# Performance work log

Hardware: AMD Instinct MI355X
Metric: run time of the kernel (lower is better)

The kernel has to match this reference:

```python
import jax, jax.numpy as jnp
import numpy as np

N = 100000   # nodes
E = 600000   # edges
SIZES = [128, 128, 128, 64]


def setup_inputs() -> dict:
    key = jax.random.key(0)
    ks = jax.random.split(key, 16)
    x = jax.random.normal(ks[0], (N, SIZES[0]), dtype=jnp.float32)
    edge_index = jax.random.randint(ks[1], (2, E), 0, N, dtype=jnp.int64)
    inp = {"x": x, "edge_index": edge_index}
    ki = 2
    for i in range(3):
        fin, fout = SIZES[i], SIZES[i + 1]
        s = 1.0 / np.sqrt(fin)
        inp[f"Wl{i}"] = jax.random.uniform(ks[ki], (fout, fin), jnp.float32, -s, s); ki += 1
        inp[f"bl{i}"] = jax.random.uniform(ks[ki], (fout,), jnp.float32, -s, s); ki += 1
        inp[f"Wr{i}"] = jax.random.uniform(ks[ki], (fout, fin), jnp.float32, -s, s); ki += 1
    return inp


def _sage(h, src, dst, Wl, bl, Wr):
    # PyG SAGEConv (aggr='mean'): out = lin_l(mean_{j in N(i)} x_j) + lin_r(x_i)
    msg_sum = jax.ops.segment_sum(h[src], dst, num_segments=N)          # [N, fin]
    cnt = jax.ops.segment_sum(jnp.ones((src.shape[0],), h.dtype), dst, num_segments=N)
    mean = msg_sum / jnp.maximum(cnt, 1.0)[:, None]                      # nodes w/o nbrs -> 0
    return mean @ Wl.T + bl + h @ Wr.T


def reference(x, edge_index, Wl0, bl0, Wr0, Wl1, bl1, Wr1, Wl2, bl2, Wr2):
    src, dst = edge_index[0], edge_index[1]
    h = _sage(x, src, dst, Wl0, bl0, Wr0)
    h = jax.nn.relu(h)                 # dropout p=0.0 -> identity
    h = _sage(h, src, dst, Wl1, bl1, Wr1)
    h = jax.nn.relu(h)
    h = _sage(h, src, dst, Wl2, bl2, Wr2)
    return h                            # last_layer='linear' appends nothing
```

## Files before the change

kernel.cpp:

```cpp
#include <hip/hip_runtime.h>

#define NN 100000
#define NE 600000
constexpr int FIN = 128;
constexpr int SCAN_BLOCKS = (NN + 255) / 256;

typedef __attribute__((ext_vector_type(8))) short bf16x8;
typedef __attribute__((ext_vector_type(4))) float f32x4;

__device__ __forceinline__ unsigned packbf2(float a, float b) {
  unsigned ua = __float_as_uint(a); ua += 0x7FFFu + ((ua >> 16) & 1u);
  unsigned ub = __float_as_uint(b); ub += 0x7FFFu + ((ub >> 16) & 1u);
  return (ua >> 16) | (ub & 0xFFFF0000u);
}
__device__ __forceinline__ float lo16f(unsigned u) { return __uint_as_float(u << 16); }
__device__ __forceinline__ float hi16f(unsigned u) { return __uint_as_float(u & 0xFFFF0000u); }

__device__ __forceinline__ void acc8(float* a, const uint4& v) {
  a[0] += lo16f(v.x); a[1] += hi16f(v.x);
  a[2] += lo16f(v.y); a[3] += hi16f(v.y);
  a[4] += lo16f(v.z); a[5] += hi16f(v.z);
  a[6] += lo16f(v.w); a[7] += hi16f(v.w);
}

template <int NCT>
__device__ __forceinline__ void castw_one(int pidx, const float* __restrict__ Wl,
                                          const float* __restrict__ Wr,
                                          short* __restrict__ wpk) {
  int t = pidx & 7;
  int lane = (pidx >> 3) & 63;
  int ks = (pidx >> 9) & 1;
  int c = (pidx >> 10) & (NCT - 1);
  int chunk = pidx >> ((NCT == 8) ? 13 : 12);
  int l15 = lane & 15, lq = lane >> 4;
  int j = c * 16 + l15;
  int k = chunk * 64 + ks * 32 + lq * 8 + t;
  float v = (k < 128) ? Wl[j * 128 + k] : Wr[j * 128 + (k - 128)];
  unsigned u = __float_as_uint(v);
  u += 0x7FFFu + ((u >> 16) & 1u);
  wpk[pidx] = (short)(u >> 16);
}

__global__ __launch_bounds__(256) void k_prep(
    const float* __restrict__ Wl0, const float* __restrict__ Wr0,
    const float* __restrict__ Wl1, const float* __restrict__ Wr1,
    const float* __restrict__ Wl2, const float* __restrict__ Wr2,
    short* __restrict__ wpk_all, float4* __restrict__ dc,
    const float* __restrict__ x, short* __restrict__ xb) {
  const int b = blockIdx.x;
  if (b < 320) {
    int pidx = b * 256 + threadIdx.x;
    if (pidx < 32768) castw_one<8>(pidx, Wl0, Wr0, wpk_all);
    else if (pidx < 65536) castw_one<8>(pidx - 32768, Wl1, Wr1, wpk_all + 32768);
    else castw_one<4>(pidx - 65536, Wl2, Wr2, wpk_all + 65536);
  } else if (b < 516) {
    int i = (b - 320) * 256 + threadIdx.x;
    if (i < 2 * NN / 4) dc[i] = make_float4(0.f, 0.f, 0.f, 0.f);
  } else {
    int i = (b - 516) * 256 + threadIdx.x;
    if (i < NN * FIN / 8) {
      const float4 v0 = *reinterpret_cast<const float4*>(x + (size_t)i * 8);
      const float4 v1 = *reinterpret_cast<const float4*>(x + (size_t)i * 8 + 4);
      uint4 o;
      o.x = packbf2(v0.x, v0.y);
      o.y = packbf2(v0.z, v0.w);
      o.z = packbf2(v1.x, v1.y);
      o.w = packbf2(v1.z, v1.w);
      *reinterpret_cast<uint4*>(xb + (size_t)i * 8) = o;
    }
  }
}


__global__ __launch_bounds__(256) void k_count(const int* __restrict__ dst,
                                               int* __restrict__ deg) {
  int e = blockIdx.x * blockDim.x + threadIdx.x;
  if (e < NE) {
    int d = dst[e];
    if ((unsigned)d < NN) atomicAdd(&deg[d], 1);
  }
}

__global__ __launch_bounds__(256) void k_scan1(const int* __restrict__ deg,
                                               int* __restrict__ rowptr,
                                               int* __restrict__ bsum,
                                               float* __restrict__ inv) {
  __shared__ int s[256];
  int i = blockIdx.x * 256 + threadIdx.x;
  int v = (i < NN) ? deg[i] : 0;
  s[threadIdx.x] = v;
  if (i < NN) inv[i] = 1.0f / fmaxf((float)v, 1.0f);
  __syncthreads();
#pragma unroll
  for (int off = 1; off < 256; off <<= 1) {
    int t = (threadIdx.x >= off) ? s[threadIdx.x - off] : 0;
    __syncthreads();
    s[threadIdx.x] += t;
    __syncthreads();
  }
  if (i < NN) rowptr[i + 1] = s[threadIdx.x];
  if (threadIdx.x == 255) bsum[blockIdx.x] = s[255];
}

__global__ __launch_bounds__(512) void k_scan2(int* __restrict__ bsum, int nb) {
  __shared__ int s[512];
  int v = (threadIdx.x < nb) ? bsum[threadIdx.x] : 0;
  s[threadIdx.x] = v;
  __syncthreads();
#pragma unroll
  for (int off = 1; off < 512; off <<= 1) {
    int t = (threadIdx.x >= off) ? s[threadIdx.x - off] : 0;
    __syncthreads();
    s[threadIdx.x] += t;
    __syncthreads();
  }
  if (threadIdx.x < nb) bsum[threadIdx.x] = s[threadIdx.x];
}

__global__ __launch_bounds__(256) void k_scan3(const int* __restrict__ bsum,
                                               int* __restrict__ rowptr) {
  int i = blockIdx.x * 256 + threadIdx.x;
  if (i < NN && blockIdx.x > 0) rowptr[i + 1] += bsum[blockIdx.x - 1];
  if (i == 0) rowptr[0] = 0;
}

__global__ __launch_bounds__(256) void k_fill(const int* __restrict__ src,
                                              const int* __restrict__ dst,
                                              const int* __restrict__ rowptr,
                                              int* __restrict__ cursor,
                                              int* __restrict__ adj) {
  int e = blockIdx.x * blockDim.x + threadIdx.x;
  if (e < NE) {
    int d = dst[e];
    int s = src[e];
    if ((unsigned)d < NN && (unsigned)s < NN) {
      int pos = atomicAdd(&cursor[d], 1);
      adj[rowptr[d] + pos] = s;
    }
  }
}

__global__ __launch_bounds__(256, 8) void k_gather2(
    const int* __restrict__ rowptr, const int* __restrict__ adj,
    const short* __restrict__ hb, const float* __restrict__ inv,
    short* __restrict__ mb) {
  const int node = blockIdx.x * 16 + (threadIdx.x >> 4);
  const int l15 = threadIdx.x & 15;
  if (node >= NN) return;
  const int beg = rowptr[node];
  const int end = rowptr[node + 1];
  const float s = inv[node];
  float a[8] = {0.f, 0.f, 0.f, 0.f, 0.f, 0.f, 0.f, 0.f};
  int e = beg;
  for (; e + 3 < end; e += 4) {
    int s0 = adj[e], s1 = adj[e + 1], s2 = adj[e + 2], s3 = adj[e + 3];
    uint4 v0 = *reinterpret_cast<const uint4*>(hb + (size_t)s0 * FIN + l15 * 8);
    uint4 v1 = *reinterpret_cast<const uint4*>(hb + (size_t)s1 * FIN + l15 * 8);
    uint4 v2 = *reinterpret_cast<const uint4*>(hb + (size_t)s2 * FIN + l15 * 8);
    uint4 v3 = *reinterpret_cast<const uint4*>(hb + (size_t)s3 * FIN + l15 * 8);
    acc8(a, v0); acc8(a, v1); acc8(a, v2); acc8(a, v3);
  }
  for (; e < end; ++e) {
    uint4 v = *reinterpret_cast<const uint4*>(hb + (size_t)adj[e] * FIN + l15 * 8);
    acc8(a, v);
  }
  uint4 o;
  o.x = packbf2(a[0] * s, a[1] * s);
  o.y = packbf2(a[2] * s, a[3] * s);
  o.z = packbf2(a[4] * s, a[5] * s);
  o.w = packbf2(a[6] * s, a[7] * s);
  *reinterpret_cast<uint4*>(mb + (size_t)node * FIN + l15 * 8) = o;
}

template <int FOUT, bool RELU, bool WF32, bool WB16>
__global__ __launch_bounds__(1024, 2) void k_gemm2(
    const short* __restrict__ hb, const short* __restrict__ mb,
    const short* __restrict__ wpk, const float* __restrict__ bias,
    float* __restrict__ out, short* __restrict__ outb) {
  constexpr int NCT = FOUT / 16;
  constexpr int NFR = NCT * 4 * 2;
  __shared__ short wlds[NFR * 64 * 8];
  const int lane = threadIdx.x & 63;
  const int w = threadIdx.x >> 6;
  const int l15 = lane & 15;
  const int lq = lane >> 4;
  const int n0 = (blockIdx.x * 16 + w) * 16;
  const int row = n0 + l15;
  const bool ok = row < NN;

#pragma unroll
  for (int i = 0; i < NFR / 16; ++i) {
    int idx = i * 1024 + threadIdx.x;
    reinterpret_cast<uint4*>(wlds)[idx] =
        reinterpret_cast<const uint4*>(wpk)[idx];
  }

  bf16x8 am[4], as_[4];
  {
    const short* mp = mb + (size_t)row * FIN + lq * 8;
    const short* sp = hb + (size_t)row * FIN + lq * 8;
#pragma unroll
    for (int q = 0; q < 4; ++q) {
      const int o = (q >> 1) * 64 + (q & 1) * 32;
      if (ok) {
        am[q] = *reinterpret_cast<const bf16x8*>(mp + o);
        as_[q] = *reinterpret_cast<const bf16x8*>(sp + o);
      } else {
#pragma unroll
        for (int i = 0; i < 8; ++i) { am[q][i] = 0; as_[q][i] = 0; }
      }
    }
  }

  __syncthreads();

  f32x4 acc[NCT];
#pragma unroll
  for (int c = 0; c < NCT; ++c)
#pragma unroll
    for (int q = 0; q < 4; ++q) acc[c][q] = 0.f;

#pragma unroll
  for (int chunk = 0; chunk < 4; ++chunk) {
    const bf16x8 a0 = (chunk < 2) ? am[chunk * 2 + 0] : as_[(chunk - 2) * 2 + 0];
    const bf16x8 a1 = (chunk < 2) ? am[chunk * 2 + 1] : as_[(chunk - 2) * 2 + 1];
#pragma unroll
    for (int c = 0; c < NCT; ++c) {
      const bf16x8 b0 = *reinterpret_cast<const bf16x8*>(
          &wlds[(((chunk * NCT + c) * 2 + 0) * 64 + lane) * 8]);
      const bf16x8 b1 = *reinterpret_cast<const bf16x8*>(
          &wlds[(((chunk * NCT + c) * 2 + 1) * 64 + lane) * 8]);
      acc[c] = __builtin_amdgcn_mfma_f32_16x16x32_bf16(b0, a0, acc[c], 0, 0, 0);
      acc[c] = __builtin_amdgcn_mfma_f32_16x16x32_bf16(b1, a1, acc[c], 0, 0, 0);
    }
  }

#pragma unroll
  for (int c = 0; c < NCT; ++c) {
    const f32x4 bb = *reinterpret_cast<const f32x4*>(bias + c * 16 + lq * 4);
    if (ok) {
      f32x4 v = acc[c] + bb;
      if (RELU) {
#pragma unroll
        for (int q = 0; q < 4; ++q) v[q] = fmaxf(v[q], 0.f);
      }
      if (WF32)
        *reinterpret_cast<f32x4*>(out + (size_t)row * FOUT + c * 16 + lq * 4) = v;
      if (WB16) {
        uint2 o;
        o.x = packbf2(v[0], v[1]);
        o.y = packbf2(v[2], v[3]);
        *reinterpret_cast<uint2*>(outb + (size_t)row * FOUT + c * 16 + lq * 4) = o;
      }
    }
  }
}


static inline size_t align512(size_t x) { return (x + 511) & ~(size_t)511; }

extern "C" void kernel_launch(void* const* d_in, const int* in_sizes, int n_in,
                              void* d_out, int out_size, void* d_ws, size_t ws_size,
                              hipStream_t stream) {
  const float* x   = (const float*)d_in[0];
  const int*   ei  = (const int*)d_in[1];
  const float* Wl0 = (const float*)d_in[2];
  const float* bl0 = (const float*)d_in[3];
  const float* Wr0 = (const float*)d_in[4];
  const float* Wl1 = (const float*)d_in[5];
  const float* bl1 = (const float*)d_in[6];
  const float* Wr1 = (const float*)d_in[7];
  const float* Wl2 = (const float*)d_in[8];
  const float* bl2 = (const float*)d_in[9];
  const float* Wr2 = (const float*)d_in[10];
  float* out = (float*)d_out;

  char* ws = (char*)d_ws;
  size_t off = 0;
  float* inv     = (float*)(ws + off); off = align512(off + (size_t)NN * 4);
  short* xb      = (short*)(ws + off); off = align512(off + (size_t)NN * FIN * 2);
  short* hb1     = (short*)(ws + off); off = align512(off + (size_t)NN * FIN * 2);
  short* hb2     = (short*)(ws + off); off = align512(off + (size_t)NN * FIN * 2);
  short* mb      = (short*)(ws + off); off = align512(off + (size_t)NN * FIN * 2);
  short* wpk_all = (short*)(ws + off); off = align512(off + (size_t)(32768 + 32768 + 16384) * 2);
  int*   deg     = (int*)(ws + off);
  int*   cursor  = deg + NN;           off = align512(off + (size_t)2 * NN * 4);
  int*   rowptr  = (int*)(ws + off);   off = align512(off + (size_t)(NN + 1) * 4);
  int*   bsum    = (int*)(ws + off);   off = align512(off + (size_t)SCAN_BLOCKS * 4);
  int*   adj     = (int*)(ws + off);   off = align512(off + (size_t)NE * 4);

  short* wpk0 = wpk_all;
  short* wpk1 = wpk_all + 32768;
  short* wpk2 = wpk_all + 65536;

  const int* srcp = ei;
  const int* dstp = ei + NE;

  const int gather_blocks = (NN + 15) / 16;
  const int gemm_blocks = (NN + 255) / 256;
  const int prep_blocks = 320 + 196 + 6250;

  k_prep<<<prep_blocks, 256, 0, stream>>>(Wl0, Wr0, Wl1, Wr1, Wl2, Wr2,
                                          wpk_all, (float4*)deg, x, xb);

  k_count<<<(NE + 255) / 256, 256, 0, stream>>>(dstp, deg);
  k_scan1<<<SCAN_BLOCKS, 256, 0, stream>>>(deg, rowptr, bsum, inv);
  k_scan2<<<1, 512, 0, stream>>>(bsum, SCAN_BLOCKS);
  k_scan3<<<SCAN_BLOCKS, 256, 0, stream>>>(bsum, rowptr);
  k_fill<<<(NE + 255) / 256, 256, 0, stream>>>(srcp, dstp, rowptr, cursor, adj);

  k_gather2<<<gather_blocks, 256, 0, stream>>>(rowptr, adj, xb, inv, mb);
  k_gemm2<128, true, false, true><<<gemm_blocks, 1024, 0, stream>>>(
      xb, mb, wpk0, bl0, nullptr, hb1);

  k_gather2<<<gather_blocks, 256, 0, stream>>>(rowptr, adj, hb1, inv, mb);
  k_gemm2<128, true, false, true><<<gemm_blocks, 1024, 0, stream>>>(
      hb1, mb, wpk1, bl1, nullptr, hb2);

  k_gather2<<<gather_blocks, 256, 0, stream>>>(rowptr, adj, hb2, inv, mb);
  k_gemm2<64, false, true, false><<<gemm_blocks, 1024, 0, stream>>>(
      hb2, mb, wpk2, bl2, out, nullptr);
}
```

Measured before the change: 224.2 us.

## Replace three-pass scan with atomic block allocation and fold degree count into prep

The per-node degree count moves into the prep kernel, and zeroing moves to a memset. The three-kernel prefix scan becomes one kernel: each block scans its degrees locally and reserves a contiguous range with a single atomicAdd on a global cursor. The gather now reads start plus degree instead of rowptr pairs. This removes several small launches and their serial dependencies. In exchange, adjacency segments are placed in nondeterministic order and the memset adds an extra operation.

```diff
diff --git a/kernel.cpp b/kernel.cpp
--- a/kernel.cpp
+++ b/kernel.cpp
@@ -3,7 +3,10 @@
 #define NN 100000
 #define NE 600000
 constexpr int FIN = 128;
-constexpr int SCAN_BLOCKS = (NN + 255) / 256;
+constexpr int COUNT_BLOCKS = (NE + 255) / 256;
+constexpr int PACK_BLOCKS = 320;
+constexpr int CAST_BLOCKS = (NN * FIN / 8 + 255) / 256;
+constexpr int ALLOC_BLOCKS = (NN + 255) / 256;
 
 typedef __attribute__((ext_vector_type(8))) short bf16x8;
 typedef __attribute__((ext_vector_type(4))) float f32x4;
@@ -42,22 +45,26 @@
 }
 
 __global__ __launch_bounds__(256) void k_prep(
+    const int* __restrict__ dst, int* __restrict__ deg,
     const float* __restrict__ Wl0, const float* __restrict__ Wr0,
     const float* __restrict__ Wl1, const float* __restrict__ Wr1,
     const float* __restrict__ Wl2, const float* __restrict__ Wr2,
-    short* __restrict__ wpk_all, float4* __restrict__ dc,
-    const float* __restrict__ x, short* __restrict__ xb) {
+    short* __restrict__ wpk_all, const float* __restrict__ x,
+    short* __restrict__ xb) {
   const int b = blockIdx.x;
-  if (b < 320) {
-    int pidx = b * 256 + threadIdx.x;
+  if (b < COUNT_BLOCKS) {
+    int e = b * 256 + threadIdx.x;
+    if (e < NE) {
+      int d = dst[e];
+      if ((unsigned)d < NN) atomicAdd(&deg[d], 1);
+    }
+  } else if (b < COUNT_BLOCKS + PACK_BLOCKS) {
+    int pidx = (b - COUNT_BLOCKS) * 256 + threadIdx.x;
     if (pidx < 32768) castw_one<8>(pidx, Wl0, Wr0, wpk_all);
     else if (pidx < 65536) castw_one<8>(pidx - 32768, Wl1, Wr1, wpk_all + 32768);
     else castw_one<4>(pidx - 65536, Wl2, Wr2, wpk_all + 65536);
-  } else if (b < 516) {
-    int i = (b - 320) * 256 + threadIdx.x;
-    if (i < 2 * NN / 4) dc[i] = make_float4(0.f, 0.f, 0.f, 0.f);
   } else {
-    int i = (b - 516) * 256 + threadIdx.x;
+    int i = (b - COUNT_BLOCKS - PACK_BLOCKS) * 256 + threadIdx.x;
     if (i < NN * FIN / 8) {
       const float4 v0 = *reinterpret_cast<const float4*>(x + (size_t)i * 8);
       const float4 v1 = *reinterpret_cast<const float4*>(x + (size_t)i * 8 + 4);
@@ -71,25 +78,15 @@
   }
 }
 
-
-__global__ __launch_bounds__(256) void k_count(const int* __restrict__ dst,
-                                               int* __restrict__ deg) {
-  int e = blockIdx.x * blockDim.x + threadIdx.x;
-  if (e < NE) {
-    int d = dst[e];
-    if ((unsigned)d < NN) atomicAdd(&deg[d], 1);
-  }
-}
-
-__global__ __launch_bounds__(256) void k_scan1(const int* __restrict__ deg,
-                                               int* __restrict__ rowptr,
-                                               int* __restrict__ bsum,
-                                               float* __restrict__ inv) {
+__global__ __launch_bounds__(256) void k_alloc(const int* __restrict__ deg,
+                                               int* __restrict__ start,
+                                               float* __restrict__ inv,
+                                               int* __restrict__ gcur) {
   __shared__ int s[256];
-  int i = blockIdx.x * 256 + threadIdx.x;
-  int v = (i < NN) ? deg[i] : 0;
+  __shared__ int base;
+  const int i = blockIdx.x * 256 + threadIdx.x;
+  const int v = (i < NN) ? deg[i] : 0;
   s[threadIdx.x] = v;
-  if (i < NN) inv[i] = 1.0f / fmaxf((float)v, 1.0f);
   __syncthreads();
 #pragma unroll
   for (int off = 1; off < 256; off <<= 1) {
@@ -98,57 +95,39 @@
     s[threadIdx.x] += t;
     __syncthreads();
   }
-  if (i < NN) rowptr[i + 1] = s[threadIdx.x];
-  if (threadIdx.x == 255) bsum[blockIdx.x] = s[255];
-}
-
-__global__ __launch_bounds__(512) void k_scan2(int* __restrict__ bsum, int nb) {
-  __shared__ int s[512];
-  int v = (threadIdx.x < nb) ? bsum[threadIdx.x] : 0;
-  s[threadIdx.x] = v;
+  if (threadIdx.x == 255) base = atomicAdd(gcur, s[255]);
   __syncthreads();
-#pragma unroll
-  for (int off = 1; off < 512; off <<= 1) {
-    int t = (threadIdx.x >= off) ? s[threadIdx.x - off] : 0;
-    __syncthreads();
-    s[threadIdx.x] += t;
-    __syncthreads();
-  }
-  if (threadIdx.x < nb) bsum[threadIdx.x] = s[threadIdx.x];
-}
-
-__global__ __launch_bounds__(256) void k_scan3(const int* __restrict__ bsum,
-                                               int* __restrict__ rowptr) {
-  int i = blockIdx.x * 256 + threadIdx.x;
-  if (i < NN && blockIdx.x > 0) rowptr[i + 1] += bsum[blockIdx.x - 1];
-  if (i == 0) rowptr[0] = 0;
+  if (i < NN) {
+    start[i] = base + s[threadIdx.x] - v;
+    inv[i] = 1.0f / fmaxf((float)v, 1.0f);
+  }
 }
 
 __global__ __launch_bounds__(256) void k_fill(const int* __restrict__ src,
                                               const int* __restrict__ dst,
-                                              const int* __restrict__ rowptr,
-                                              int* __restrict__ cursor,
+                                              const int* __restrict__ start,
+                                              int* __restrict__ fillcur,
                                               int* __restrict__ adj) {
   int e = blockIdx.x * blockDim.x + threadIdx.x;
   if (e < NE) {
     int d = dst[e];
     int s = src[e];
     if ((unsigned)d < NN && (unsigned)s < NN) {
-      int pos = atomicAdd(&cursor[d], 1);
-      adj[rowptr[d] + pos] = s;
+      int pos = atomicAdd(&fillcur[d], 1);
+      adj[start[d] + pos] = s;
     }
   }
 }
 
 __global__ __launch_bounds__(256, 8) void k_gather2(
-    const int* __restrict__ rowptr, const int* __restrict__ adj,
-    const short* __restrict__ hb, const float* __restrict__ inv,
-    short* __restrict__ mb) {
+    const int* __restrict__ start, const int* __restrict__ deg,
+    const int* __restrict__ adj, const short* __restrict__ hb,
+    const float* __restrict__ inv, short* __restrict__ mb) {
   const int node = blockIdx.x * 16 + (threadIdx.x >> 4);
   const int l15 = threadIdx.x & 15;
   if (node >= NN) return;
-  const int beg = rowptr[node];
-  const int end = rowptr[node + 1];
+  const int beg = start[node];
+  const int end = beg + deg[node];
   const float s = inv[node];
   float a[8] = {0.f, 0.f, 0.f, 0.f, 0.f, 0.f, 0.f, 0.f};
   int e = beg;
@@ -284,9 +263,9 @@
   short* mb      = (short*)(ws + off); off = align512(off + (size_t)NN * FIN * 2);
   short* wpk_all = (short*)(ws + off); off = align512(off + (size_t)(32768 + 32768 + 16384) * 2);
   int*   deg     = (int*)(ws + off);
-  int*   cursor  = deg + NN;           off = align512(off + (size_t)2 * NN * 4);
-  int*   rowptr  = (int*)(ws + off);   off = align512(off + (size_t)(NN + 1) * 4);
-  int*   bsum    = (int*)(ws + off);   off = align512(off + (size_t)SCAN_BLOCKS * 4);
+  int*   fillcur = deg + NN;
+  int*   gcur    = deg + 2 * NN;       off = align512(off + ((size_t)2 * NN + 1) * 4);
+  int*   start   = (int*)(ws + off);   off = align512(off + (size_t)NN * 4);
   int*   adj     = (int*)(ws + off);   off = align512(off + (size_t)NE * 4);
 
   short* wpk0 = wpk_all;
@@ -298,26 +277,25 @@
 
   const int gather_blocks = (NN + 15) / 16;
   const int gemm_blocks = (NN + 255) / 256;
-  const int prep_blocks = 320 + 196 + 6250;
-
-  k_prep<<<prep_blocks, 256, 0, stream>>>(Wl0, Wr0, Wl1, Wr1, Wl2, Wr2,
-                                          wpk_all, (float4*)deg, x, xb);
-
-  k_count<<<(NE + 255) / 256, 256, 0, stream>>>(dstp, deg);
-  k_scan1<<<SCAN_BLOCKS, 256, 0, stream>>>(deg, rowptr, bsum, inv);
-  k_scan2<<<1, 512, 0, stream>>>(bsum, SCAN_BLOCKS);
-  k_scan3<<<SCAN_BLOCKS, 256, 0, stream>>>(bsum, rowptr);
-  k_fill<<<(NE + 255) / 256, 256, 0, stream>>>(srcp, dstp, rowptr, cursor, adj);
-
-  k_gather2<<<gather_blocks, 256, 0, stream>>>(rowptr, adj, xb, inv, mb);
+  const int prep_blocks = COUNT_BLOCKS + PACK_BLOCKS + CAST_BLOCKS;
+
+  hipMemsetAsync(deg, 0, ((size_t)2 * NN + 1) * sizeof(int), stream);
+
+  k_prep<<<prep_blocks, 256, 0, stream>>>(dstp, deg, Wl0, Wr0, Wl1, Wr1,
+                                          Wl2, Wr2, wpk_all, x, xb);
+
+  k_alloc<<<ALLOC_BLOCKS, 256, 0, stream>>>(deg, start, inv, gcur);
+  k_fill<<<COUNT_BLOCKS, 256, 0, stream>>>(srcp, dstp, start, fillcur, adj);
+
+  k_gather2<<<gather_blocks, 256, 0, stream>>>(start, deg, adj, xb, inv, mb);
   k_gemm2<128, true, false, true><<<gemm_blocks, 1024, 0, stream>>>(
       xb, mb, wpk0, bl0, nullptr, hb1);
 
-  k_gather2<<<gather_blocks, 256, 0, stream>>>(rowptr, adj, hb1, inv, mb);
+  k_gather2<<<gather_blocks, 256, 0, stream>>>(start, deg, adj, hb1, inv, mb);
   k_gemm2<128, true, false, true><<<gemm_blocks, 1024, 0, stream>>>(
       hb1, mb, wpk1, bl1, nullptr, hb2);
 
-  k_gather2<<<gather_blocks, 256, 0, stream>>>(rowptr, adj, hb2, inv, mb);
+  k_gather2<<<gather_blocks, 256, 0, stream>>>(start, deg, adj, hb2, inv, mb);
   k_gemm2<64, false, true, false><<<gemm_blocks, 1024, 0, stream>>>(
       hb2, mb, wpk2, bl2, out, nullptr);
 }
```

Measured after the change: 228.5 us. Within noise of the previous version (+1.9%).
